# Kernel tuning notes

Measured on AMD Instinct MI355X. Metric: run time of the kernel, lower is better.

The kernel has to match this reference:

```python
import jax, jax.numpy as jnp
import numpy as np

H = 16
D_MODEL = 1024
D_K = D_MODEL // H


def setup_inputs() -> dict:
    key = jax.random.key(0)
    ks = jax.random.split(key, 11)
    B, S = 4, 2048
    scale = 1.0 / np.sqrt(D_MODEL)
    inp = {
        "query": jax.random.normal(ks[0], (B, S, D_MODEL), dtype=jnp.float32),
        "key": jax.random.normal(ks[1], (B, S, D_MODEL), dtype=jnp.float32),
        "value": jax.random.normal(ks[2], (B, S, D_MODEL), dtype=jnp.float32),
        "Wq": jax.random.normal(ks[3], (D_MODEL, D_MODEL), dtype=jnp.float32) * scale,
        "bq": jnp.zeros((D_MODEL,), dtype=jnp.float32),
        "Wk": jax.random.normal(ks[4], (D_MODEL, D_MODEL), dtype=jnp.float32) * scale,
        "bk": jnp.zeros((D_MODEL,), dtype=jnp.float32),
        "Wv": jax.random.normal(ks[5], (D_MODEL, D_MODEL), dtype=jnp.float32) * scale,
        "bv": jnp.zeros((D_MODEL,), dtype=jnp.float32),
        "Wo": jax.random.normal(ks[6], (D_MODEL, D_MODEL), dtype=jnp.float32) * scale,
        "bo": jnp.zeros((D_MODEL,), dtype=jnp.float32),
    }
    return inp


def reference(query, key, value, Wq, bq, Wk, bk, Wv, bv, Wo, bo):
    B, S, _ = query.shape

    def proj(x, W, b):
        # nn.Linear: x @ W.T + b, then split heads -> [B, H, S, D_K]
        y = jnp.einsum("bsd,ed->bse", x, W) + b
        return y.reshape(B, S, H, D_K).transpose(0, 2, 1, 3)

    q = proj(query, Wq, bq)
    k = proj(key, Wk, bk)
    v = proj(value, Wv, bv)

    scores = jnp.einsum("bhqd,bhkd->bhqk", q, k) / jnp.sqrt(jnp.float32(D_K))
    attn = jax.nn.softmax(scores, axis=-1)
    out = jnp.einsum("bhqk,bhkd->bhqd", attn, v)  # [B,H,S,D_K]
    out = out.transpose(0, 2, 1, 3).reshape(B, S, H * D_K)
    # final linear (dropout disabled in eval / deterministic reference)
    return jnp.einsum("bsd,ed->bse", out, Wo) + bo
```

## Files before the change

### kernel.cpp

```cpp
#include <hip/hip_runtime.h>
#include <stdint.h>

typedef __attribute__((ext_vector_type(8))) short short8;
typedef __attribute__((ext_vector_type(4))) float floatx4;
typedef __attribute__((ext_vector_type(16))) float floatx16;

#define DEV __device__ __forceinline__

DEV unsigned short f2bf(float x) {
  unsigned u = __float_as_uint(x);
  u += 0x7fffu + ((u >> 16) & 1u);
  return (unsigned short)(u >> 16);
}

DEV unsigned pkbf(float hi, float lo) {
  return __builtin_amdgcn_perm(__float_as_uint(hi) + 0x8000u,
                               __float_as_uint(lo) + 0x8000u, 0x07060302u);
}

DEV unsigned cvtpk(float a, float b) {
  unsigned r;
  asm("v_cvt_pk_bf16_f32 %0, %1, %2" : "=v"(r) : "v"(a), "v"(b));
  return r;
}

DEV short8 pack4(unsigned a0, unsigned a1, unsigned b0, unsigned b1) {
  union { unsigned u[4]; short8 s; } t;
  t.u[0] = a0; t.u[1] = a1; t.u[2] = b0; t.u[3] = b1;
  return t.s;
}

DEV void load_lds16(const unsigned short* g, unsigned short* l) {
  __builtin_amdgcn_global_load_lds(
      (const __attribute__((address_space(1))) void*)g,
      (__attribute__((address_space(3))) void*)l, 16, 0, 0);
}

DEV void lds_fence() { asm volatile("" ::: "memory"); }

#define ASM_VMCNT(n) asm volatile("s_waitcnt vmcnt(" #n ")" ::: "memory")
DEV void sched_fence() { __builtin_amdgcn_sched_barrier(0); }

__global__ void cvt_all(const float* __restrict__ Wq, const float* __restrict__ Wk,
                        const float* __restrict__ Wv, const float* __restrict__ Wo,
                        const float* __restrict__ Xq, const float* __restrict__ Xk,
                        const float* __restrict__ Xv,
                        unsigned short* __restrict__ Wb, unsigned short* __restrict__ XqB,
                        unsigned short* __restrict__ XkB, unsigned short* __restrict__ XvB) {
  int bid = blockIdx.x;
  const float* src;
  unsigned short* dst;
  int off;
  if (bid < 4096) {
    int sel = bid >> 10;
    src = sel == 0 ? Wq : sel == 1 ? Wk : sel == 2 ? Wv : Wo;
    dst = Wb + (size_t)sel * 1048576;
    off = bid & 1023;
  } else {
    bid -= 4096;
    int sel = bid >> 13;
    src = sel == 0 ? Xq : sel == 1 ? Xk : Xv;
    dst = sel == 0 ? XqB : sel == 1 ? XkB : XvB;
    off = bid & 8191;
  }
  int i = (off * 256 + threadIdx.x) * 4;
  float4 v = *(const float4*)(src + i);
  uint2 o;
  o.x = pkbf(v.y, v.x);
  o.y = pkbf(v.w, v.z);
  *(uint2*)(dst + i) = o;
}

#define SCQ (0.125f * 1.44269504089f)
__global__ __launch_bounds__(256, 3) void qkv_gemm(
    const unsigned short* __restrict__ XqB, const unsigned short* __restrict__ XkB,
    const unsigned short* __restrict__ XvB,
    const unsigned short* __restrict__ Wb,
    const float* __restrict__ bq, const float* __restrict__ bk, const float* __restrict__ bv,
    unsigned short* __restrict__ Qp, unsigned short* __restrict__ Kp,
    unsigned short* __restrict__ VTp) {
  __shared__ alignas(16) unsigned short Xs[3][128 * 32];
  __shared__ alignas(16) unsigned short Ws[3][128 * 32];
  const int z = blockIdx.z;
  const unsigned short* X = z == 0 ? XqB : z == 1 ? XkB : XvB;
  const unsigned short* W = Wb + (size_t)z * 1048576;
  const float* bias = z == 0 ? bq : z == 1 ? bk : bv;

  const int tid = threadIdx.x;
  const int lane = tid & 63, wave = tid >> 6;
  const int lcol = lane & 15, quad = lane >> 4;
  const int n2 = blockIdx.x + 8 * blockIdx.y;
  const int xcd = n2 & 7, ii = n2 >> 3;
  const int wo = (ii >> 3) * 128;
  const int xo = (xcd * 8 + (ii & 7)) * 128;
  const int wm = (wave & 1) * 64;
  const int wn = (wave >> 1) * 64;

  floatx4 acc[4][4];
  for (int mi = 0; mi < 4; ++mi)
    for (int ni = 0; ni < 4; ++ni)
      for (int r = 0; r < 4; ++r) acc[mi][ni][r] = 0.f;

  auto stage = [&](int kt, int buf) {
    const int k0 = kt * 32;
    int c = tid;
    load_lds16(W + (size_t)(wo + (c >> 2)) * 1024 + k0 + (c & 3) * 8, Ws[buf] + c * 8);
    load_lds16(X + (size_t)(xo + (c >> 2)) * 1024 + k0 + (c & 3) * 8, Xs[buf] + c * 8);
    c = tid + 256;
    load_lds16(W + (size_t)(wo + (c >> 2)) * 1024 + k0 + (c & 3) * 8, Ws[buf] + c * 8);
    load_lds16(X + (size_t)(xo + (c >> 2)) * 1024 + k0 + (c & 3) * 8, Xs[buf] + c * 8);
  };

  stage(0, 0);
  stage(1, 1);
  int cur = 0;
  for (int kt = 0; kt < 32; ++kt) {
    sched_fence();
    ASM_VMCNT(4);
    __builtin_amdgcn_s_barrier();
    sched_fence();
    int nb = cur + 2; if (nb >= 3) nb -= 3;
    stage((kt + 2) & 31, nb);
    const unsigned short* Ab = (z < 2) ? Ws[cur] : Xs[cur];
    const unsigned short* Bb = (z < 2) ? Xs[cur] : Ws[cur];
    short8 af[4], bfr[4];
#pragma unroll
    for (int mi = 0; mi < 4; ++mi)
      af[mi] = *(const short8*)(Ab + (wm + mi * 16 + lcol) * 32 + quad * 8);
#pragma unroll
    for (int ni = 0; ni < 4; ++ni)
      bfr[ni] = *(const short8*)(Bb + (wn + ni * 16 + lcol) * 32 + quad * 8);
#pragma unroll
    for (int mi = 0; mi < 4; ++mi)
#pragma unroll
      for (int ni = 0; ni < 4; ++ni)
        acc[mi][ni] = __builtin_amdgcn_mfma_f32_16x16x32_bf16(af[mi], bfr[ni], acc[mi][ni], 0, 0, 0);
    cur = (cur == 2) ? 0 : cur + 1;
  }

  if (z < 2) {
    unsigned short* Out = z == 0 ? Qp : Kp;
    const float scl = z == 0 ? SCQ : 1.f;
#pragma unroll
    for (int mi = 0; mi < 4; ++mi) {
      int dbase = wo + wm + mi * 16 + quad * 4;
      float4 bv4 = *(const float4*)(bias + dbase);
      int h = dbase >> 6, dk = dbase & 63;
#pragma unroll
      for (int ni = 0; ni < 4; ++ni) {
        int sg = xo + wn + ni * 16 + lcol;
        int bb = sg >> 11, ss = sg & 2047;
        uint2 o;
        o.x = pkbf((acc[mi][ni][1] + bv4.y) * scl, (acc[mi][ni][0] + bv4.x) * scl);
        o.y = pkbf((acc[mi][ni][3] + bv4.w) * scl, (acc[mi][ni][2] + bv4.z) * scl);
        *(uint2*)(Out + ((size_t)(bb * 16 + h) * 2048 + ss) * 64 + dk) = o;
      }
    }
  } else {
#pragma unroll
    for (int ni = 0; ni < 4; ++ni) {
      int dg = wo + wn + ni * 16 + lcol;
      float bvx = bias[dg];
      int h = dg >> 6, dk = dg & 63;
#pragma unroll
      for (int mi = 0; mi < 4; ++mi) {
        int sbase = xo + wm + mi * 16 + quad * 4;
        int bb = sbase >> 11, ss = sbase & 2047;
        uint2 o;
        o.x = pkbf(acc[mi][ni][1] + bvx, acc[mi][ni][0] + bvx);
        o.y = pkbf(acc[mi][ni][3] + bvx, acc[mi][ni][2] + bvx);
        *(uint2*)(VTp + ((size_t)(bb * 16 + h) * 64 + dk) * 2048 + ss) = o;
      }
    }
  }
}

__global__ __launch_bounds__(256, 3) void gemm_o(
    const unsigned short* __restrict__ A, const unsigned short* __restrict__ Bw,
    const float* __restrict__ bias, float* __restrict__ Out) {
  __shared__ alignas(16) unsigned short Cs[3][128 * 32];
  __shared__ alignas(16) unsigned short Wos[3][128 * 32];
  const int tid = threadIdx.x;
  const int lane = tid & 63, wave = tid >> 6;
  const int lcol = lane & 15, quad = lane >> 4;
  const int n2 = blockIdx.x + 8 * blockIdx.y;
  const int xcd = n2 & 7, ii = n2 >> 3;
  const int co = (ii >> 3) * 128;
  const int so = (xcd * 8 + (ii & 7)) * 128;
  const int wm = (wave & 1) * 64;
  const int wn = (wave >> 1) * 64;

  floatx4 acc[4][4];
  for (int mi = 0; mi < 4; ++mi)
    for (int ni = 0; ni < 4; ++ni)
      for (int r = 0; r < 4; ++r) acc[mi][ni][r] = 0.f;

  auto stage = [&](int kt, int buf) {
    const int k0 = kt * 32;
    int c = tid;
    load_lds16(Bw + (size_t)(co + (c >> 2)) * 1024 + k0 + (c & 3) * 8, Wos[buf] + c * 8);
    load_lds16(A  + (size_t)(so + (c >> 2)) * 1024 + k0 + (c & 3) * 8, Cs[buf] + c * 8);
    c = tid + 256;
    load_lds16(Bw + (size_t)(co + (c >> 2)) * 1024 + k0 + (c & 3) * 8, Wos[buf] + c * 8);
    load_lds16(A  + (size_t)(so + (c >> 2)) * 1024 + k0 + (c & 3) * 8, Cs[buf] + c * 8);
  };

  stage(0, 0);
  stage(1, 1);
  int cur = 0;
  for (int kt = 0; kt < 32; ++kt) {
    sched_fence();
    ASM_VMCNT(4);
    __builtin_amdgcn_s_barrier();
    sched_fence();
    int nb = cur + 2; if (nb >= 3) nb -= 3;
    stage((kt + 2) & 31, nb);
    short8 af[4], bfr[4];
#pragma unroll
    for (int mi = 0; mi < 4; ++mi)
      af[mi] = *(const short8*)(Wos[cur] + (wm + mi * 16 + lcol) * 32 + quad * 8);
#pragma unroll
    for (int ni = 0; ni < 4; ++ni)
      bfr[ni] = *(const short8*)(Cs[cur] + (wn + ni * 16 + lcol) * 32 + quad * 8);
#pragma unroll
    for (int mi = 0; mi < 4; ++mi)
#pragma unroll
      for (int ni = 0; ni < 4; ++ni)
        acc[mi][ni] = __builtin_amdgcn_mfma_f32_16x16x32_bf16(af[mi], bfr[ni], acc[mi][ni], 0, 0, 0);
    cur = (cur == 2) ? 0 : cur + 1;
  }
#pragma unroll
  for (int mi = 0; mi < 4; ++mi) {
    int cb = co + wm + mi * 16 + quad * 4;
    float4 bv4 = *(const float4*)(bias + cb);
#pragma unroll
    for (int ni = 0; ni < 4; ++ni) {
      int sg = so + wn + ni * 16 + lcol;
      float4 o;
      o.x = acc[mi][ni][0] + bv4.x;
      o.y = acc[mi][ni][1] + bv4.y;
      o.z = acc[mi][ni][2] + bv4.z;
      o.w = acc[mi][ni][3] + bv4.w;
      *(float4*)(Out + (size_t)sg * 1024 + cb) = o;
    }
  }
}

__global__ __launch_bounds__(256, 3) void attn_kernel(
    const unsigned short* __restrict__ Qp, const unsigned short* __restrict__ Kp,
    const unsigned short* __restrict__ VTp, unsigned short* __restrict__ Ctx) {
  __shared__ alignas(16) unsigned short Ks[3][64 * 64];
  __shared__ alignas(16) unsigned short Vt[3][64 * 64];

  const int tid = threadIdx.x;
  const int lane = tid & 63, wave = tid >> 6;
  const int l31 = lane & 31, hh = lane >> 5;
  const int wq = wave * 32;
  const int n = blockIdx.x + 16 * (blockIdx.y + 16 * blockIdx.z);
  const int xcd = n & 7, ii = n >> 3;
  const int hb = xcd * 8 + (ii & 7);
  const int qt = ii >> 3;
  const size_t bh = (size_t)hb * 2048 * 64;
  const int b = hb >> 4;
  const unsigned short* Qb = Qp + bh + (size_t)qt * 128 * 64;
  const unsigned short* Kb = Kp + bh;
  const unsigned short* VTb = VTp + bh;

  short8 qf[4];
#pragma unroll
  for (int st = 0; st < 4; ++st)
    qf[st] = *(const short8*)(Qb + (wq + l31) * 64 + st * 16 + hh * 8);

  auto stageK = [&](int jt, int buf) {
#pragma unroll
    for (int i = 0; i < 2; ++i) {
      int p = tid + i * 256;
      int kr = p >> 3, kj = p & 7;
      load_lds16(Kb + (size_t)jt * 4096 + kr * 64 + ((kj ^ (kr & 7)) * 8), Ks[buf] + p * 8);
    }
  };
  auto stageV = [&](int jt, int buf) {
#pragma unroll
    for (int i = 0; i < 2; ++i) {
      int p = tid + i * 256;
      int vr = p >> 3, vj = p & 7;
      load_lds16(VTb + (size_t)vr * 2048 + jt * 64 + ((vj ^ (vr & 7)) * 8), Vt[buf] + p * 8);
    }
  };

  stageK(0, 0); stageV(0, 0);
  stageK(1, 1); stageV(1, 1);
  __syncthreads();

  short8 ones;
#pragma unroll
  for (int j = 0; j < 8; ++j) ones[j] = (short)0x3f80;

  float M = -1e30f;
  floatx16 Oacc[2], OaccL;
#pragma unroll
  for (int r = 0; r < 16; ++r) { Oacc[0][r] = 0.f; Oacc[1][r] = 0.f; OaccL[r] = 0.f; }

  int cur = 0;
  for (int jt = 0; jt < 32; ++jt) {
    int nb = cur + 2; if (nb >= 3) nb -= 3;
    const int jn = (jt + 2) & 31;
    stageK(jn, nb);
    stageV(jn, nb);

    const unsigned short* Kc = Ks[cur];
    floatx16 sacc[2];
#pragma unroll
    for (int r = 0; r < 16; ++r) { sacc[0][r] = 0.f; sacc[1][r] = 0.f; }
#pragma unroll
    for (int st = 0; st < 4; ++st)
#pragma unroll
      for (int mk = 0; mk < 2; ++mk) {
        int row = mk * 32 + l31;
        short8 kf = *(const short8*)(Kc + row * 64 + (((2 * st + hh) ^ (row & 7)) * 8));
        sacc[mk] = __builtin_amdgcn_mfma_f32_32x32x16_bf16(kf, qf[st], sacc[mk], 0, 0, 0);
      }

    float t8[8];
#pragma unroll
    for (int r = 0; r < 8; ++r)
      t8[r] = fmaxf(fmaxf(sacc[0][r], sacc[0][r + 8]), fmaxf(sacc[1][r], sacc[1][r + 8]));
    float t4a = fmaxf(t8[0], t8[4]), t4b = fmaxf(t8[1], t8[5]);
    float t4c = fmaxf(t8[2], t8[6]), t4d = fmaxf(t8[3], t8[7]);
    float mloc = fmaxf(fmaxf(t4a, t4b), fmaxf(t4c, t4d));
    float m2 = fmaxf(mloc, __shfl_xor(mloc, 32));

    const int skip = __all(m2 <= M + 8.f);
    if (!skip) {
      float mnew = fmaxf(M, m2);
      float alpha = exp2f(M - mnew);
      M = mnew;
#pragma unroll
      for (int r = 0; r < 16; ++r) {
        int srcl = (r & 3) + 8 * (r >> 2) + hh * 4;
        float ar = __shfl(alpha, srcl);
        Oacc[0][r] *= ar;
        Oacc[1][r] *= ar;
        OaccL[r] *= ar;
      }
    }
#pragma unroll
    for (int mk = 0; mk < 2; ++mk)
#pragma unroll
      for (int r = 0; r < 16; ++r) sacc[mk][r] = exp2f(sacc[mk][r] - M);

    unsigned wpk[2][4][2];
#pragma unroll
    for (int mk = 0; mk < 2; ++mk)
#pragma unroll
      for (int c = 0; c < 4; ++c) {
        wpk[mk][c][0] = cvtpk(sacc[mk][4 * c + 0], sacc[mk][4 * c + 1]);
        wpk[mk][c][1] = cvtpk(sacc[mk][4 * c + 2], sacc[mk][4 * c + 3]);
      }

    const unsigned short* Vc = Vt[cur];
#pragma unroll
    for (int kk = 0; kk < 4; ++kk) {
      const int e = kk & 1, mk = kk >> 1;
      unsigned a0 = wpk[mk][2 * e][0], b0 = wpk[mk][2 * e + 1][0];
      unsigned a1 = wpk[mk][2 * e][1], b1 = wpk[mk][2 * e + 1][1];
      asm("v_permlane32_swap_b32 %0, %1" : "+v"(a0), "+v"(b0));
      asm("v_permlane32_swap_b32 %0, %1" : "+v"(a1), "+v"(b1));
      short8 pa = pack4(a0, a1, b0, b1);
#pragma unroll
      for (int nd = 0; nd < 2; ++nd) {
        int row = nd * 32 + l31;
        short8 vf = *(const short8*)(Vc + row * 64 + (((2 * kk + hh) ^ (row & 7)) * 8));
        Oacc[nd] = __builtin_amdgcn_mfma_f32_32x32x16_bf16(pa, vf, Oacc[nd], 0, 0, 0);
      }
      OaccL = __builtin_amdgcn_mfma_f32_32x32x16_bf16(pa, ones, OaccL, 0, 0, 0);
    }

    sched_fence();
    ASM_VMCNT(4);
    __builtin_amdgcn_s_barrier();
    sched_fence();
    cur = (cur == 2) ? 0 : cur + 1;
  }

  ASM_VMCNT(0);
  __syncthreads();
  unsigned short* Obuf = &Ks[0][0];
  float linv[16];
#pragma unroll
  for (int r = 0; r < 16; ++r) linv[r] = 1.f / OaccL[r];
#pragma unroll
  for (int nd = 0; nd < 2; ++nd)
#pragma unroll
    for (int r = 0; r < 16; ++r) {
      int q = wq + (r & 3) + 8 * (r >> 2) + hh * 4;
      int d = nd * 32 + l31;
      Obuf[q * 64 + (((d >> 3) ^ (q & 7)) * 8) + (d & 7)] = f2bf(Oacc[nd][r] * linv[r]);
    }
  __syncthreads();
#pragma unroll
  for (int i = 0; i < 4; ++i) {
    int c = tid + i * 256;
    int row = c >> 3, pj = c & 7;
    uint4 v = *(const uint4*)(Obuf + row * 64 + ((pj ^ (row & 7)) * 8));
    *(uint4*)(Ctx + ((size_t)(b * 2048 + qt * 128 + row)) * 1024 + (hb & 15) * 64 + pj * 8) = v;
  }
}

extern "C" void kernel_launch(void* const* d_in, const int* in_sizes, int n_in,
                              void* d_out, int out_size, void* d_ws, size_t ws_size,
                              hipStream_t stream) {
  const float* query = (const float*)d_in[0];
  const float* key_  = (const float*)d_in[1];
  const float* value = (const float*)d_in[2];
  const float* Wq = (const float*)d_in[3];
  const float* bq = (const float*)d_in[4];
  const float* Wk = (const float*)d_in[5];
  const float* bk = (const float*)d_in[6];
  const float* Wv = (const float*)d_in[7];
  const float* bv = (const float*)d_in[8];
  const float* Wo = (const float*)d_in[9];
  const float* bo = (const float*)d_in[10];

  char* w = (char*)d_ws;
  unsigned short* Wb  = (unsigned short*)w; w += (size_t)4 * 1024 * 1024 * 2;
  unsigned short* Qp  = (unsigned short*)w; w += (size_t)8192 * 1024 * 2;
  unsigned short* Kp  = (unsigned short*)w; w += (size_t)8192 * 1024 * 2;
  unsigned short* VTp = (unsigned short*)w; w += (size_t)8192 * 1024 * 2;
  unsigned short* Ctx = (unsigned short*)w; w += (size_t)8192 * 1024 * 2;

  unsigned short* XqB = (unsigned short*)d_out;
  unsigned short* XkB = (unsigned short*)d_out + (size_t)8192 * 1024;
  unsigned short* XvB = Ctx;

  cvt_all<<<28672, 256, 0, stream>>>(Wq, Wk, Wv, Wo, query, key_, value,
                                     Wb, XqB, XkB, XvB);

  qkv_gemm<<<dim3(8, 64, 3), 256, 0, stream>>>(XqB, XkB, XvB, Wb,
                                               bq, bk, bv, Qp, Kp, VTp);

  attn_kernel<<<dim3(16, 16, 4), 256, 0, stream>>>(Qp, Kp, VTp, Ctx);

  gemm_o<<<dim3(8, 64), 256, 0, stream>>>(Ctx, Wb + (size_t)3 * 1048576, bo, (float*)d_out);
}
```

Baseline: 375.6 us.

## Enlarge GEMM tiles to 128x256 with 8 waves, swizzled LDS, split-phase pipeline

Both projection GEMMs move to 512-thread blocks covering 128x256 output tiles, so each weight tile is reused across twice as many rows. LDS staging now uses an XOR swizzle to cut bank conflicts. Each k-step is split into two barrier-separated phases that interleave async loads with MFMA bursts under raised wave priority. The attention kernel shrinks V buffering to double-buffered with a shorter prefetch distance, cutting LDS use to allow higher occupancy, at the risk of exposing V load latency.

```diff
diff --git a/kernel.cpp b/kernel.cpp
--- a/kernel.cpp
+++ b/kernel.cpp
@@ -35,8 +35,6 @@
       (const __attribute__((address_space(1))) void*)g,
       (__attribute__((address_space(3))) void*)l, 16, 0, 0);
 }
-
-DEV void lds_fence() { asm volatile("" ::: "memory"); }
 
 #define ASM_VMCNT(n) asm volatile("s_waitcnt vmcnt(" #n ")" ::: "memory")
 DEV void sched_fence() { __builtin_amdgcn_sched_barrier(0); }
@@ -71,15 +69,19 @@
   *(uint2*)(dst + i) = o;
 }
 
+DEV short8 fragld(const unsigned short* buf, int row, int quad) {
+  return *(const short8*)(buf + row * 32 + ((quad ^ ((row >> 1) & 3)) * 8));
+}
+
 #define SCQ (0.125f * 1.44269504089f)
-__global__ __launch_bounds__(256, 3) void qkv_gemm(
+__global__ __launch_bounds__(512, 4) void qkv_gemm(
     const unsigned short* __restrict__ XqB, const unsigned short* __restrict__ XkB,
     const unsigned short* __restrict__ XvB,
     const unsigned short* __restrict__ Wb,
     const float* __restrict__ bq, const float* __restrict__ bk, const float* __restrict__ bv,
     unsigned short* __restrict__ Qp, unsigned short* __restrict__ Kp,
     unsigned short* __restrict__ VTp) {
-  __shared__ alignas(16) unsigned short Xs[3][128 * 32];
+  __shared__ alignas(16) unsigned short Xs[3][256 * 32];
   __shared__ alignas(16) unsigned short Ws[3][128 * 32];
   const int z = blockIdx.z;
   const unsigned short* X = z == 0 ? XqB : z == 1 ? XkB : XvB;
@@ -91,50 +93,84 @@
   const int lcol = lane & 15, quad = lane >> 4;
   const int n2 = blockIdx.x + 8 * blockIdx.y;
   const int xcd = n2 & 7, ii = n2 >> 3;
-  const int wo = (ii >> 3) * 128;
-  const int xo = (xcd * 8 + (ii & 7)) * 128;
-  const int wm = (wave & 1) * 64;
-  const int wn = (wave >> 1) * 64;
+  const int wo = (ii & 7) * 128;
+  const int xo = (xcd * 4 + (ii >> 3)) * 256;
+  const int wd = (wave & 1) * 64;
+  const int ws_ = (wave >> 1) * 64;
+  const int wm = (z < 2) ? wd : ws_;
+  const int wn = (z < 2) ? ws_ : wd;
 
   floatx4 acc[4][4];
   for (int mi = 0; mi < 4; ++mi)
     for (int ni = 0; ni < 4; ++ni)
       for (int r = 0; r < 4; ++r) acc[mi][ni][r] = 0.f;
 
-  auto stage = [&](int kt, int buf) {
+  auto stageX = [&](int kt, int buf) {
+    const int k0 = kt * 32;
+#pragma unroll
+    for (int l = 0; l < 2; ++l) {
+      int c = tid + l * 512;
+      int row = c >> 2, ch = c & 3;
+      load_lds16(X + (size_t)(xo + row) * 1024 + k0 + ((ch ^ ((row >> 1) & 3)) * 8),
+                 Xs[buf] + c * 8);
+    }
+  };
+  auto stageW = [&](int kt, int buf) {
     const int k0 = kt * 32;
     int c = tid;
-    load_lds16(W + (size_t)(wo + (c >> 2)) * 1024 + k0 + (c & 3) * 8, Ws[buf] + c * 8);
-    load_lds16(X + (size_t)(xo + (c >> 2)) * 1024 + k0 + (c & 3) * 8, Xs[buf] + c * 8);
-    c = tid + 256;
-    load_lds16(W + (size_t)(wo + (c >> 2)) * 1024 + k0 + (c & 3) * 8, Ws[buf] + c * 8);
-    load_lds16(X + (size_t)(xo + (c >> 2)) * 1024 + k0 + (c & 3) * 8, Xs[buf] + c * 8);
+    int row = c >> 2, ch = c & 3;
+    load_lds16(W + (size_t)(wo + row) * 1024 + k0 + ((ch ^ ((row >> 1) & 3)) * 8),
+               Ws[buf] + c * 8);
   };
 
-  stage(0, 0);
-  stage(1, 1);
+  stageX(0, 0); stageW(0, 0);
+  stageX(1, 1); stageW(1, 1);
+  __syncthreads();
+
   int cur = 0;
   for (int kt = 0; kt < 32; ++kt) {
     sched_fence();
-    ASM_VMCNT(4);
+    ASM_VMCNT(3);
     __builtin_amdgcn_s_barrier();
     sched_fence();
     int nb = cur + 2; if (nb >= 3) nb -= 3;
-    stage((kt + 2) & 31, nb);
+    const int kn = (kt + 2) & 31;
     const unsigned short* Ab = (z < 2) ? Ws[cur] : Xs[cur];
     const unsigned short* Bb = (z < 2) ? Xs[cur] : Ws[cur];
-    short8 af[4], bfr[4];
-#pragma unroll
-    for (int mi = 0; mi < 4; ++mi)
-      af[mi] = *(const short8*)(Ab + (wm + mi * 16 + lcol) * 32 + quad * 8);
-#pragma unroll
-    for (int ni = 0; ni < 4; ++ni)
-      bfr[ni] = *(const short8*)(Bb + (wn + ni * 16 + lcol) * 32 + quad * 8);
-#pragma unroll
-    for (int mi = 0; mi < 4; ++mi)
-#pragma unroll
-      for (int ni = 0; ni < 4; ++ni)
-        acc[mi][ni] = __builtin_amdgcn_mfma_f32_16x16x32_bf16(af[mi], bfr[ni], acc[mi][ni], 0, 0, 0);
+
+    short8 a0 = fragld(Ab, wm + lcol, quad);
+    short8 a1 = fragld(Ab, wm + 16 + lcol, quad);
+    short8 b0 = fragld(Bb, wn + lcol, quad);
+    short8 b1 = fragld(Bb, wn + 16 + lcol, quad);
+    short8 b2 = fragld(Bb, wn + 32 + lcol, quad);
+    short8 b3 = fragld(Bb, wn + 48 + lcol, quad);
+    stageX(kn, nb);
+    __builtin_amdgcn_s_setprio(1);
+    acc[0][0] = __builtin_amdgcn_mfma_f32_16x16x32_bf16(a0, b0, acc[0][0], 0, 0, 0);
+    acc[0][1] = __builtin_amdgcn_mfma_f32_16x16x32_bf16(a0, b1, acc[0][1], 0, 0, 0);
+    acc[0][2] = __builtin_amdgcn_mfma_f32_16x16x32_bf16(a0, b2, acc[0][2], 0, 0, 0);
+    acc[0][3] = __builtin_amdgcn_mfma_f32_16x16x32_bf16(a0, b3, acc[0][3], 0, 0, 0);
+    acc[1][0] = __builtin_amdgcn_mfma_f32_16x16x32_bf16(a1, b0, acc[1][0], 0, 0, 0);
+    acc[1][1] = __builtin_amdgcn_mfma_f32_16x16x32_bf16(a1, b1, acc[1][1], 0, 0, 0);
+    acc[1][2] = __builtin_amdgcn_mfma_f32_16x16x32_bf16(a1, b2, acc[1][2], 0, 0, 0);
+    acc[1][3] = __builtin_amdgcn_mfma_f32_16x16x32_bf16(a1, b3, acc[1][3], 0, 0, 0);
+    __builtin_amdgcn_s_setprio(0);
+    sched_fence();
+    __builtin_amdgcn_s_barrier();
+    sched_fence();
+    short8 a2 = fragld(Ab, wm + 32 + lcol, quad);
+    short8 a3 = fragld(Ab, wm + 48 + lcol, quad);
+    stageW(kn, nb);
+    __builtin_amdgcn_s_setprio(1);
+    acc[2][0] = __builtin_amdgcn_mfma_f32_16x16x32_bf16(a2, b0, acc[2][0], 0, 0, 0);
+    acc[2][1] = __builtin_amdgcn_mfma_f32_16x16x32_bf16(a2, b1, acc[2][1], 0, 0, 0);
+    acc[2][2] = __builtin_amdgcn_mfma_f32_16x16x32_bf16(a2, b2, acc[2][2], 0, 0, 0);
+    acc[2][3] = __builtin_amdgcn_mfma_f32_16x16x32_bf16(a2, b3, acc[2][3], 0, 0, 0);
+    acc[3][0] = __builtin_amdgcn_mfma_f32_16x16x32_bf16(a3, b0, acc[3][0], 0, 0, 0);
+    acc[3][1] = __builtin_amdgcn_mfma_f32_16x16x32_bf16(a3, b1, acc[3][1], 0, 0, 0);
+    acc[3][2] = __builtin_amdgcn_mfma_f32_16x16x32_bf16(a3, b2, acc[3][2], 0, 0, 0);
+    acc[3][3] = __builtin_amdgcn_mfma_f32_16x16x32_bf16(a3, b3, acc[3][3], 0, 0, 0);
+    __builtin_amdgcn_s_setprio(0);
     cur = (cur == 2) ? 0 : cur + 1;
   }
 
@@ -175,18 +211,18 @@
   }
 }
 
-__global__ __launch_bounds__(256, 3) void gemm_o(
+__global__ __launch_bounds__(512, 4) void gemm_o(
     const unsigned short* __restrict__ A, const unsigned short* __restrict__ Bw,
     const float* __restrict__ bias, float* __restrict__ Out) {
-  __shared__ alignas(16) unsigned short Cs[3][128 * 32];
+  __shared__ alignas(16) unsigned short Cs[3][256 * 32];
   __shared__ alignas(16) unsigned short Wos[3][128 * 32];
   const int tid = threadIdx.x;
   const int lane = tid & 63, wave = tid >> 6;
   const int lcol = lane & 15, quad = lane >> 4;
   const int n2 = blockIdx.x + 8 * blockIdx.y;
   const int xcd = n2 & 7, ii = n2 >> 3;
-  const int co = (ii >> 3) * 128;
-  const int so = (xcd * 8 + (ii & 7)) * 128;
+  const int co = (ii & 7) * 128;
+  const int so = (xcd * 4 + (ii >> 3)) * 256;
   const int wm = (wave & 1) * 64;
   const int wn = (wave >> 1) * 64;
 
@@ -195,38 +231,72 @@
     for (int ni = 0; ni < 4; ++ni)
       for (int r = 0; r < 4; ++r) acc[mi][ni][r] = 0.f;
 
-  auto stage = [&](int kt, int buf) {
+  auto stageC = [&](int kt, int buf) {
+    const int k0 = kt * 32;
+#pragma unroll
+    for (int l = 0; l < 2; ++l) {
+      int c = tid + l * 512;
+      int row = c >> 2, ch = c & 3;
+      load_lds16(A + (size_t)(so + row) * 1024 + k0 + ((ch ^ ((row >> 1) & 3)) * 8),
+                 Cs[buf] + c * 8);
+    }
+  };
+  auto stageB = [&](int kt, int buf) {
     const int k0 = kt * 32;
     int c = tid;
-    load_lds16(Bw + (size_t)(co + (c >> 2)) * 1024 + k0 + (c & 3) * 8, Wos[buf] + c * 8);
-    load_lds16(A  + (size_t)(so + (c >> 2)) * 1024 + k0 + (c & 3) * 8, Cs[buf] + c * 8);
-    c = tid + 256;
-    load_lds16(Bw + (size_t)(co + (c >> 2)) * 1024 + k0 + (c & 3) * 8, Wos[buf] + c * 8);
-    load_lds16(A  + (size_t)(so + (c >> 2)) * 1024 + k0 + (c & 3) * 8, Cs[buf] + c * 8);
+    int row = c >> 2, ch = c & 3;
+    load_lds16(Bw + (size_t)(co + row) * 1024 + k0 + ((ch ^ ((row >> 1) & 3)) * 8),
+               Wos[buf] + c * 8);
   };
 
-  stage(0, 0);
-  stage(1, 1);
+  stageC(0, 0); stageB(0, 0);
+  stageC(1, 1); stageB(1, 1);
+  __syncthreads();
+
   int cur = 0;
   for (int kt = 0; kt < 32; ++kt) {
     sched_fence();
-    ASM_VMCNT(4);
+    ASM_VMCNT(3);
     __builtin_amdgcn_s_barrier();
     sched_fence();
     int nb = cur + 2; if (nb >= 3) nb -= 3;
-    stage((kt + 2) & 31, nb);
-    short8 af[4], bfr[4];
-#pragma unroll
-    for (int mi = 0; mi < 4; ++mi)
-      af[mi] = *(const short8*)(Wos[cur] + (wm + mi * 16 + lcol) * 32 + quad * 8);
-#pragma unroll
-    for (int ni = 0; ni < 4; ++ni)
-      bfr[ni] = *(const short8*)(Cs[cur] + (wn + ni * 16 + lcol) * 32 + quad * 8);
-#pragma unroll
-    for (int mi = 0; mi < 4; ++mi)
-#pragma unroll
-      for (int ni = 0; ni < 4; ++ni)
-        acc[mi][ni] = __builtin_amdgcn_mfma_f32_16x16x32_bf16(af[mi], bfr[ni], acc[mi][ni], 0, 0, 0);
+    const int kn = (kt + 2) & 31;
+    const unsigned short* Ab = Wos[cur];
+    const unsigned short* Bb = Cs[cur];
+
+    short8 a0 = fragld(Ab, wm + lcol, quad);
+    short8 a1 = fragld(Ab, wm + 16 + lcol, quad);
+    short8 b0 = fragld(Bb, wn + lcol, quad);
+    short8 b1 = fragld(Bb, wn + 16 + lcol, quad);
+    short8 b2 = fragld(Bb, wn + 32 + lcol, quad);
+    short8 b3 = fragld(Bb, wn + 48 + lcol, quad);
+    stageC(kn, nb);
+    __builtin_amdgcn_s_setprio(1);
+    acc[0][0] = __builtin_amdgcn_mfma_f32_16x16x32_bf16(a0, b0, acc[0][0], 0, 0, 0);
+    acc[0][1] = __builtin_amdgcn_mfma_f32_16x16x32_bf16(a0, b1, acc[0][1], 0, 0, 0);
+    acc[0][2] = __builtin_amdgcn_mfma_f32_16x16x32_bf16(a0, b2, acc[0][2], 0, 0, 0);
+    acc[0][3] = __builtin_amdgcn_mfma_f32_16x16x32_bf16(a0, b3, acc[0][3], 0, 0, 0);
+    acc[1][0] = __builtin_amdgcn_mfma_f32_16x16x32_bf16(a1, b0, acc[1][0], 0, 0, 0);
+    acc[1][1] = __builtin_amdgcn_mfma_f32_16x16x32_bf16(a1, b1, acc[1][1], 0, 0, 0);
+    acc[1][2] = __builtin_amdgcn_mfma_f32_16x16x32_bf16(a1, b2, acc[1][2], 0, 0, 0);
+    acc[1][3] = __builtin_amdgcn_mfma_f32_16x16x32_bf16(a1, b3, acc[1][3], 0, 0, 0);
+    __builtin_amdgcn_s_setprio(0);
+    sched_fence();
+    __builtin_amdgcn_s_barrier();
+    sched_fence();
+    short8 a2 = fragld(Ab, wm + 32 + lcol, quad);
+    short8 a3 = fragld(Ab, wm + 48 + lcol, quad);
+    stageB(kn, nb);
+    __builtin_amdgcn_s_setprio(1);
+    acc[2][0] = __builtin_amdgcn_mfma_f32_16x16x32_bf16(a2, b0, acc[2][0], 0, 0, 0);
+    acc[2][1] = __builtin_amdgcn_mfma_f32_16x16x32_bf16(a2, b1, acc[2][1], 0, 0, 0);
+    acc[2][2] = __builtin_amdgcn_mfma_f32_16x16x32_bf16(a2, b2, acc[2][2], 0, 0, 0);
+    acc[2][3] = __builtin_amdgcn_mfma_f32_16x16x32_bf16(a2, b3, acc[2][3], 0, 0, 0);
+    acc[3][0] = __builtin_amdgcn_mfma_f32_16x16x32_bf16(a3, b0, acc[3][0], 0, 0, 0);
+    acc[3][1] = __builtin_amdgcn_mfma_f32_16x16x32_bf16(a3, b1, acc[3][1], 0, 0, 0);
+    acc[3][2] = __builtin_amdgcn_mfma_f32_16x16x32_bf16(a3, b2, acc[3][2], 0, 0, 0);
+    acc[3][3] = __builtin_amdgcn_mfma_f32_16x16x32_bf16(a3, b3, acc[3][3], 0, 0, 0);
+    __builtin_amdgcn_s_setprio(0);
     cur = (cur == 2) ? 0 : cur + 1;
   }
 #pragma unroll
@@ -246,11 +316,11 @@
   }
 }
 
-__global__ __launch_bounds__(256, 3) void attn_kernel(
+__global__ __launch_bounds__(256, 4) void attn_kernel(
     const unsigned short* __restrict__ Qp, const unsigned short* __restrict__ Kp,
     const unsigned short* __restrict__ VTp, unsigned short* __restrict__ Ctx) {
   __shared__ alignas(16) unsigned short Ks[3][64 * 64];
-  __shared__ alignas(16) unsigned short Vt[3][64 * 64];
+  __shared__ alignas(16) unsigned short Vt[2][64 * 64];
 
   const int tid = threadIdx.x;
   const int lane = tid & 63, wave = tid >> 6;
@@ -288,8 +358,9 @@
     }
   };
 
-  stageK(0, 0); stageV(0, 0);
-  stageK(1, 1); stageV(1, 1);
+  stageV(0, 0);
+  stageK(0, 0);
+  stageK(1, 1);
   __syncthreads();
 
   short8 ones;
@@ -301,14 +372,13 @@
 #pragma unroll
   for (int r = 0; r < 16; ++r) { Oacc[0][r] = 0.f; Oacc[1][r] = 0.f; OaccL[r] = 0.f; }
 
-  int cur = 0;
+  int kcur = 0;
   for (int jt = 0; jt < 32; ++jt) {
-    int nb = cur + 2; if (nb >= 3) nb -= 3;
-    const int jn = (jt + 2) & 31;
-    stageK(jn, nb);
-    stageV(jn, nb);
-
-    const unsigned short* Kc = Ks[cur];
+    stageV((jt + 1) & 31, (jt + 1) & 1);
+    int knb = kcur + 2; if (knb >= 3) knb -= 3;
+    stageK((jt + 2) & 31, knb);
+
+    const unsigned short* Kc = Ks[kcur];
     floatx16 sacc[2];
 #pragma unroll
     for (int r = 0; r < 16; ++r) { sacc[0][r] = 0.f; sacc[1][r] = 0.f; }
@@ -358,7 +428,7 @@
         wpk[mk][c][1] = cvtpk(sacc[mk][4 * c + 2], sacc[mk][4 * c + 3]);
       }
 
-    const unsigned short* Vc = Vt[cur];
+    const unsigned short* Vc = Vt[jt & 1];
 #pragma unroll
     for (int kk = 0; kk < 4; ++kk) {
       const int e = kk & 1, mk = kk >> 1;
@@ -377,10 +447,10 @@
     }
 
     sched_fence();
-    ASM_VMCNT(4);
+    ASM_VMCNT(2);
     __builtin_amdgcn_s_barrier();
     sched_fence();
-    cur = (cur == 2) ? 0 : cur + 1;
+    kcur = (kcur == 2) ? 0 : kcur + 1;
   }
 
   ASM_VMCNT(0);
@@ -436,10 +506,10 @@
   cvt_all<<<28672, 256, 0, stream>>>(Wq, Wk, Wv, Wo, query, key_, value,
                                      Wb, XqB, XkB, XvB);
 
-  qkv_gemm<<<dim3(8, 64, 3), 256, 0, stream>>>(XqB, XkB, XvB, Wb,
+  qkv_gemm<<<dim3(8, 32, 3), 512, 0, stream>>>(XqB, XkB, XvB, Wb,
                                                bq, bk, bv, Qp, Kp, VTp);
 
   attn_kernel<<<dim3(16, 16, 4), 256, 0, stream>>>(Qp, Kp, VTp, Ctx);
 
-  gemm_o<<<dim3(8, 64), 256, 0, stream>>>(Ctx, Wb + (size_t)3 * 1048576, bo, (float*)d_out);
-}
+  gemm_o<<<dim3(8, 32), 512, 0, stream>>>(Ctx, Wb + (size_t)3 * 1048576, bo, (float*)d_out);
+}
```

Result: slower. 399.2 us (+6.3%).
